# Kernel optimization log

Measured on AMD Instinct MI355X. Metric: run time of the kernel, lower is better.

## Reference

```python
import jax, jax.numpy as jnp
import numpy as np

N_NODES = 50000
N_EDGES = 800000
D = 64  # ndim_in = edim = n_hidden = n_out


def _glorot(key, shape):
    fan_in = shape[0]
    return jax.random.normal(key, shape, dtype=jnp.float32) / jnp.sqrt(jnp.float32(fan_in))


def setup_inputs() -> dict:
    key = jax.random.key(0)
    ks = jax.random.split(key, 10)
    return {
        "nfeats": jax.random.normal(ks[0], (N_NODES, D), dtype=jnp.float32),
        "efeats": jax.random.normal(ks[1], (N_EDGES, D), dtype=jnp.float32),
        "src": jax.random.randint(ks[2], (N_EDGES,), 0, N_NODES),
        "dst": jax.random.randint(ks[3], (N_EDGES,), 0, N_NODES),
        "wa0": _glorot(ks[4], (3 * D, D)), "ba0": jnp.zeros((D,), jnp.float32),
        "we0": _glorot(ks[5], (2 * D, D)), "be0": jnp.zeros((D,), jnp.float32),
        "wa1": _glorot(ks[6], (3 * D, D)), "ba1": jnp.zeros((D,), jnp.float32),
        "we1": _glorot(ks[7], (2 * D, D)), "be1": jnp.zeros((D,), jnp.float32),
    }


def _layer(h_nodes, h_edges, src, dst, wa, ba, we, be):
    n = h_nodes.shape[0]
    # per-edge message: concat(src node feat, edge feat)  [E, ndim+edim]
    msg = jnp.concatenate([h_nodes[src], h_edges], axis=1)
    # mean-reduce messages onto destination nodes (DGL fn.mean -> 0 if no in-edges)
    msum = jax.ops.segment_sum(msg, dst, num_segments=n)
    cnt = jax.ops.segment_sum(jnp.ones((msg.shape[0],), msg.dtype), dst, num_segments=n)
    h_neigh = msum / jnp.maximum(cnt, 1.0)[:, None]
    x_apply = jnp.concatenate([h_nodes, h_neigh], axis=1)  # [N, 2*ndim+edim]
    h_nodes_new = jax.nn.relu(x_apply @ wa + ba)
    # edge update: concat endpoint node outputs, then MLP
    edge_in = jnp.concatenate([h_nodes_new[src], h_nodes_new[dst]], axis=1)
    h_edges_new = jax.nn.relu(edge_in @ we + be)
    return h_nodes_new, h_edges_new


def reference(nfeats, efeats, src, dst, wa0, ba0, we0, be0, wa1, ba1, we1, be1):
    h_n, h_e = _layer(nfeats, efeats, src, dst, wa0, ba0, we0, be0)
    h_n, h_e = _layer(h_n, h_e, src, dst, wa1, ba1, we1, be1)
    return (h_n, h_e)
```

## Files before the change

kernel.cpp:

```cpp
#include <hip/hip_runtime.h>

#define NN 50000
#define NE 800000
#define CAP 64

typedef float f32x4 __attribute__((ext_vector_type(4)));
typedef unsigned short u16x4 __attribute__((ext_vector_type(4)));
typedef _Float16 f16x8 __attribute__((ext_vector_type(8)));

__device__ __forceinline__ float h_to_f(unsigned short u) {
    union { unsigned short s; _Float16 h; } c; c.s = u; return (float)c.h;
}
__device__ __forceinline__ unsigned short f_to_h(float f) {
    union { unsigned short s; _Float16 h; } c; c.h = (_Float16)f; return c.s;
}

__global__ __launch_bounds__(256) void k_prep(
    const float* __restrict__ nfeats, unsigned short* __restrict__ nfh)
{
    size_t b = ((size_t)blockIdx.x * 256 + threadIdx.x) * 4;
    f32x4 v = *(const f32x4*)(nfeats + b);
    u16x4 o;
#pragma unroll
    for (int j = 0; j < 4; ++j) o[j] = f_to_h(v[j]);
    *(u16x4*)(nfh + b) = o;
}

__global__ __launch_bounds__(256) void k_bucket(
    const int* __restrict__ src, const int* __restrict__ dst,
    int* __restrict__ fill, int2* __restrict__ epair)
{
    int e = blockIdx.x * 256 + threadIdx.x;
    int d = dst[e];
    int pos = atomicAdd(&fill[d], 1);
    if (pos < CAP) epair[(size_t)d * CAP + pos] = make_int2(src[e], e);
}

template <bool L2>
__global__ __launch_bounds__(256) void k_layer(
    const void* __restrict__ hin_,
    const unsigned short* __restrict__ nfh, const float* __restrict__ efeats,
    const unsigned short* __restrict__ P0g, const float* __restrict__ B0,
    const int* __restrict__ fill, const int2* __restrict__ epair,
    const float* __restrict__ wa, const float* __restrict__ ba,
    const float* __restrict__ we, const float* __restrict__ be,
    float* __restrict__ hout, unsigned short* __restrict__ pack,
    float* __restrict__ b32, unsigned short* __restrict__ a16,
    unsigned short* __restrict__ b16)
{
    __shared__ __align__(16) char smem[51200];
    __shared__ float ba_sh[64], be_sh[64];
    _Float16* xh  = (_Float16*)smem;
    _Float16* wah = (_Float16*)(smem + 25600);
    _Float16* heh = (_Float16*)smem;
    _Float16* weh = (_Float16*)(smem + 9216);

    int tid = threadIdx.x;
    int t0 = blockIdx.x * 64;
    if (tid < 64) { ba_sh[tid] = ba[tid]; be_sh[tid] = be[tid]; }

    for (int c = tid; c < 64 * 192; c += 256) {
        int n = c / 192, k = c - n * 192;
        wah[n * 200 + k] = (_Float16)wa[k * 64 + n];
    }
    for (int c = tid; c < 64 * 64; c += 256) {
        int rw = c >> 6, k = c & 63;
        int node = t0 + rw;
        float v = 0.f;
        if (node < NN) {
            if (L2) v = h_to_f(((const unsigned short*)hin_)[(size_t)node * 128 + k]);
            else    v = ((const float*)hin_)[(size_t)node * 64 + k];
        }
        xh[rw * 200 + k] = (_Float16)v;
    }

    int lane = tid & 63, wv = tid >> 6;
    for (int i = 0; i < 16; ++i) {
        int row = i * 4 + wv;
        int node = t0 + row;
        if (node >= NN) {
            xh[row * 200 + 64 + lane] = (_Float16)0.f;
            xh[row * 200 + 128 + lane] = (_Float16)0.f;
            continue;
        }
        int dg = fill[node];
        int nl = dg < CAP ? dg : CAP;
        int2 q = make_int2(0, 0);
        if (lane < nl) q = epair[(size_t)node * CAP + lane];
        float bB = 0.f;
        if (L2) bB = B0[(size_t)node * 64 + lane];
        float accN = 0.f, accE = 0.f;
        for (int t = 0; t < nl; t += 8) {
            int ss[8], ee[8];
#pragma unroll
            for (int u = 0; u < 8; ++u) {
                ss[u] = __shfl(q.x, t + u);
                ee[u] = __shfl(q.y, t + u);
            }
            float nv[8], ev[8];
#pragma unroll
            for (int u = 0; u < 8; ++u) {
                if (L2) {
                    nv[u] = h_to_f(P0g[(size_t)ss[u] * 128 + lane]);
                    ev[u] = h_to_f(P0g[(size_t)ss[u] * 128 + 64 + lane]);
                } else {
                    nv[u] = h_to_f(nfh[(size_t)ss[u] * 64 + lane]);
                    ev[u] = efeats[(size_t)ee[u] * 64 + lane];
                }
            }
#pragma unroll
            for (int u = 0; u < 8; ++u) {
                bool ok = (t + u) < nl;
                accN += ok ? nv[u] : 0.f;
                float x = L2 ? (ev[u] + bB) : ev[u];
                if (L2) x = x > 0.f ? x : 0.f;
                accE += ok ? x : 0.f;
            }
        }
        float dinv = 1.f / (float)(dg > 1 ? dg : 1);
        xh[row * 200 + 64 + lane]  = (_Float16)(accN * dinv);
        xh[row * 200 + 128 + lane] = (_Float16)(accE * dinv);
    }
    __syncthreads();

    int l15 = lane & 15, quad = lane >> 4;

    f32x4 acc[4];
#pragma unroll
    for (int nt = 0; nt < 4; ++nt) {
        float b = ba_sh[nt * 16 + l15];
        acc[nt] = (f32x4){b, b, b, b};
    }
    const _Float16* xp = xh + (wv * 16 + l15) * 200 + quad * 8;
    const _Float16* wp = wah + l15 * 200 + quad * 8;
#pragma unroll
    for (int ks = 0; ks < 6; ++ks) {
        f16x8 a  = *(const f16x8*)(xp + ks * 32);
        f16x8 b0 = *(const f16x8*)(wp + ks * 32);
        f16x8 b1 = *(const f16x8*)(wp + 16 * 200 + ks * 32);
        f16x8 b2 = *(const f16x8*)(wp + 32 * 200 + ks * 32);
        f16x8 b3 = *(const f16x8*)(wp + 48 * 200 + ks * 32);
        acc[0] = __builtin_amdgcn_mfma_f32_16x16x32_f16(a, b0, acc[0], 0, 0, 0);
        acc[1] = __builtin_amdgcn_mfma_f32_16x16x32_f16(a, b1, acc[1], 0, 0, 0);
        acc[2] = __builtin_amdgcn_mfma_f32_16x16x32_f16(a, b2, acc[2], 0, 0, 0);
        acc[3] = __builtin_amdgcn_mfma_f32_16x16x32_f16(a, b3, acc[3], 0, 0, 0);
    }
    __syncthreads();

    for (int c = tid; c < 8192; c += 256) {
        int n = c >> 6, k = c & 63;
        float wv_ = (n < 64) ? we[k * 64 + n] : we[(size_t)(64 + k) * 64 + (n - 64)];
        weh[n * 72 + k] = (_Float16)wv_;
    }
#pragma unroll
    for (int nt = 0; nt < 4; ++nt)
#pragma unroll
        for (int r = 0; r < 4; ++r) {
            float v = acc[nt][r];
            v = v > 0.f ? v : 0.f;
            int row = wv * 16 + quad * 4 + r, col = nt * 16 + l15;
            heh[row * 72 + col] = (_Float16)v;
            int node = t0 + row;
            if (node < NN) {
                if (L2) hout[(size_t)node * 64 + col] = v;
                else    pack[(size_t)node * 128 + col] = f_to_h(v);
            }
        }
    __syncthreads();

    f32x4 acc2[8];
#pragma unroll
    for (int nt = 0; nt < 8; ++nt) {
        float b = (nt >= 4) ? be_sh[(nt - 4) * 16 + l15] : 0.f;
        acc2[nt] = (f32x4){b, b, b, b};
    }
    const _Float16* hp = heh + (wv * 16 + l15) * 72 + quad * 8;
    const _Float16* vp = weh + l15 * 72 + quad * 8;
#pragma unroll
    for (int ks = 0; ks < 2; ++ks) {
        f16x8 a = *(const f16x8*)(hp + ks * 32);
#pragma unroll
        for (int nt = 0; nt < 8; ++nt) {
            f16x8 b = *(const f16x8*)(vp + nt * 16 * 72 + ks * 32);
            acc2[nt] = __builtin_amdgcn_mfma_f32_16x16x32_f16(a, b, acc2[nt], 0, 0, 0);
        }
    }
#pragma unroll
    for (int nt = 0; nt < 8; ++nt)
#pragma unroll
        for (int r = 0; r < 4; ++r) {
            float v = acc2[nt][r];
            int row = wv * 16 + quad * 4 + r, col = (nt & 3) * 16 + l15;
            int node = t0 + row;
            if (node < NN) {
                if (nt < 4) {
                    if (L2) a16[(size_t)node * 64 + col] = f_to_h(v);
                    else    pack[(size_t)node * 128 + 64 + col] = f_to_h(v);
                } else {
                    if (L2) b16[(size_t)node * 64 + col] = f_to_h(v);
                    else    b32[(size_t)node * 64 + col] = v;
                }
            }
        }
}

__global__ __launch_bounds__(256) void k_edge_out(
    const int* __restrict__ src, const int* __restrict__ dst,
    const unsigned short* __restrict__ A, const unsigned short* __restrict__ B,
    float* __restrict__ oute)
{
    size_t g = (size_t)blockIdx.x * 256 + threadIdx.x;
    size_t e = g >> 4;
    int c = ((int)g & 15) * 4;
    if (e >= NE) return;
    int s = src[e], d = dst[e];
    u16x4 a = *(const u16x4*)(A + (size_t)s * 64 + c);
    u16x4 b = *(const u16x4*)(B + (size_t)d * 64 + c);
    f32x4 v;
#pragma unroll
    for (int j = 0; j < 4; ++j) {
        float x = h_to_f(a[j]) + h_to_f(b[j]);
        v[j] = x > 0.f ? x : 0.f;
    }
    *(f32x4*)(oute + e * 64 + c) = v;
}

extern "C" void kernel_launch(void* const* d_in, const int* in_sizes, int n_in,
                              void* d_out, int out_size, void* d_ws, size_t ws_size,
                              hipStream_t stream)
{
    const float* nfeats = (const float*)d_in[0];
    const float* efeats = (const float*)d_in[1];
    const int*   src    = (const int*)d_in[2];
    const int*   dst    = (const int*)d_in[3];
    const float* wa0 = (const float*)d_in[4];
    const float* ba0 = (const float*)d_in[5];
    const float* we0 = (const float*)d_in[6];
    const float* be0 = (const float*)d_in[7];
    const float* wa1 = (const float*)d_in[8];
    const float* ba1 = (const float*)d_in[9];
    const float* we1 = (const float*)d_in[10];
    const float* be1 = (const float*)d_in[11];

    float* out_n = (float*)d_out;
    float* out_e = out_n + (size_t)NN * 64;

    char* w = (char*)d_ws;
    int* fill = (int*)w;  w += ((size_t)NN * 4 + 255) & ~(size_t)255;
    int2* epair = (int2*)w; w += (size_t)NN * CAP * 8;
    unsigned short* nfh = (unsigned short*)w; w += (size_t)NN * 64 * 2;
    unsigned short* P0  = (unsigned short*)w; w += (size_t)NN * 128 * 2;
    float* B0 = (float*)w; w += (size_t)NN * 64 * 4;
    unsigned short* A1 = (unsigned short*)w; w += (size_t)NN * 64 * 2;
    unsigned short* B1 = (unsigned short*)w; w += (size_t)NN * 64 * 2;

    hipMemsetAsync(fill, 0, (size_t)NN * 4, stream);
    k_prep<<<3125, 256, 0, stream>>>(nfeats, nfh);
    k_bucket<<<NE / 256, 256, 0, stream>>>(src, dst, fill, epair);

    k_layer<false><<<(NN + 63) / 64, 256, 0, stream>>>(
        nfeats, nfh, efeats, nullptr, nullptr, fill, epair,
        wa0, ba0, we0, be0, nullptr, P0, B0, nullptr, nullptr);

    k_layer<true><<<(NN + 63) / 64, 256, 0, stream>>>(
        P0, nullptr, nullptr, P0, B0, fill, epair,
        wa1, ba1, we1, be1, out_n, nullptr, nullptr, A1, B1);

    k_edge_out<<<(int)((size_t)NE * 16 / 256), 256, 0, stream>>>(src, dst, A1, B1, out_e);
}
```

Before: 685.9 us.

## Pre-convert weights once, bucket fp16 edge features by destination, shrink layer tiles

Adds a one-time weight prep kernel that transposes both layers' weights to fp16 in global memory. Layer kernels now read MFMA B operands straight from global memory instead of rebuilding them in LDS in every block. The bucket kernel now also scatters each edge's features, converted to fp16, into a per-destination contiguous buffer, so layer 0's aggregation reads contiguous rows instead of random fp32 rows. Node tiles shrink from 64 to 32 rows to reduce LDS use and increase block count, at the cost of a heavier bucketing pass and an extra ~400MB workspace write for the bucketed edges.

```diff
diff --git a/kernel.cpp b/kernel.cpp
--- a/kernel.cpp
+++ b/kernel.cpp
@@ -6,6 +6,7 @@
 
 typedef float f32x4 __attribute__((ext_vector_type(4)));
 typedef unsigned short u16x4 __attribute__((ext_vector_type(4)));
+typedef unsigned short u16x8 __attribute__((ext_vector_type(8)));
 typedef _Float16 f16x8 __attribute__((ext_vector_type(8)));
 
 __device__ __forceinline__ float h_to_f(unsigned short u) {
@@ -26,44 +27,71 @@
     *(u16x4*)(nfh + b) = o;
 }
 
+__global__ __launch_bounds__(256) void k_wprep(
+    const float* __restrict__ wa0, const float* __restrict__ we0,
+    const float* __restrict__ wa1, const float* __restrict__ we1,
+    _Float16* __restrict__ wahg, _Float16* __restrict__ wehg)
+{
+    int idx = blockIdx.x * 256 + threadIdx.x;
+    int layer = idx / 20480, r = idx % 20480;
+    const float* wa = layer ? wa1 : wa0;
+    const float* we = layer ? we1 : we0;
+    if (r < 12288) {
+        int n = r / 192, k = r % 192;
+        wahg[layer * 12288 + r] = (_Float16)wa[k * 64 + n];
+    } else {
+        int r2 = r - 12288;
+        int n = r2 >> 6, k = r2 & 63;
+        float v = (n < 64) ? we[k * 64 + n] : we[(size_t)(64 + k) * 64 + (n - 64)];
+        wehg[layer * 8192 + r2] = (_Float16)v;
+    }
+}
+
 __global__ __launch_bounds__(256) void k_bucket(
     const int* __restrict__ src, const int* __restrict__ dst,
-    int* __restrict__ fill, int2* __restrict__ epair)
+    const float* __restrict__ efeats, int* __restrict__ fill,
+    int* __restrict__ sbuck, unsigned short* __restrict__ ebuck)
 {
     int e = blockIdx.x * 256 + threadIdx.x;
     int d = dst[e];
     int pos = atomicAdd(&fill[d], 1);
-    if (pos < CAP) epair[(size_t)d * CAP + pos] = make_int2(src[e], e);
+    if (pos >= CAP) return;
+    size_t slot = (size_t)d * CAP + pos;
+    sbuck[slot] = src[e];
+    const float* er = efeats + (size_t)e * 64;
+    unsigned short* ew = ebuck + slot * 64;
+#pragma unroll
+    for (int j = 0; j < 8; ++j) {
+        f32x4 a = *(const f32x4*)(er + j * 8);
+        f32x4 b = *(const f32x4*)(er + j * 8 + 4);
+        u16x8 o;
+#pragma unroll
+        for (int q = 0; q < 4; ++q) { o[q] = f_to_h(a[q]); o[4 + q] = f_to_h(b[q]); }
+        *(u16x8*)(ew + j * 8) = o;
+    }
 }
 
 template <bool L2>
 __global__ __launch_bounds__(256) void k_layer(
     const void* __restrict__ hin_,
-    const unsigned short* __restrict__ nfh, const float* __restrict__ efeats,
+    const unsigned short* __restrict__ nfh, const unsigned short* __restrict__ ebuck,
     const unsigned short* __restrict__ P0g, const float* __restrict__ B0,
-    const int* __restrict__ fill, const int2* __restrict__ epair,
-    const float* __restrict__ wa, const float* __restrict__ ba,
-    const float* __restrict__ we, const float* __restrict__ be,
+    const int* __restrict__ fill, const int* __restrict__ sbuck,
+    const _Float16* __restrict__ wahg, const float* __restrict__ ba,
+    const _Float16* __restrict__ wehg, const float* __restrict__ be,
     float* __restrict__ hout, unsigned short* __restrict__ pack,
     float* __restrict__ b32, unsigned short* __restrict__ a16,
     unsigned short* __restrict__ b16)
 {
-    __shared__ __align__(16) char smem[51200];
+    __shared__ __align__(16) _Float16 xh[32 * 200];
+    _Float16* heh = xh;
     __shared__ float ba_sh[64], be_sh[64];
-    _Float16* xh  = (_Float16*)smem;
-    _Float16* wah = (_Float16*)(smem + 25600);
-    _Float16* heh = (_Float16*)smem;
-    _Float16* weh = (_Float16*)(smem + 9216);
 
     int tid = threadIdx.x;
-    int t0 = blockIdx.x * 64;
+    int t0 = blockIdx.x * 32;
     if (tid < 64) { ba_sh[tid] = ba[tid]; be_sh[tid] = be[tid]; }
 
-    for (int c = tid; c < 64 * 192; c += 256) {
-        int n = c / 192, k = c - n * 192;
-        wah[n * 200 + k] = (_Float16)wa[k * 64 + n];
-    }
-    for (int c = tid; c < 64 * 64; c += 256) {
+    for (int c = tid; c < 32 * 64; c += 256) {
         int rw = c >> 6, k = c & 63;
         int node = t0 + rw;
         float v = 0.f;
@@ -75,7 +103,7 @@
     }
 
     int lane = tid & 63, wv = tid >> 6;
-    for (int i = 0; i < 16; ++i) {
+    for (int i = 0; i < 8; ++i) {
         int row = i * 4 + wv;
         int node = t0 + row;
         if (node >= NN) {
@@ -85,18 +113,14 @@
         }
         int dg = fill[node];
         int nl = dg < CAP ? dg : CAP;
-        int2 q = make_int2(0, 0);
-        if (lane < nl) q = epair[(size_t)node * CAP + lane];
-        float bB = 0.f;
-        if (L2) bB = B0[(size_t)node * 64 + lane];
+        int sp = (lane < nl) ? sbuck[(size_t)node * CAP + lane] : 0;
+        float bB = L2 ? B0[(size_t)node * 64 + lane] : 0.f;
+        const unsigned short* eb = ebuck + (size_t)node * CAP * 64;
         float accN = 0.f, accE = 0.f;
         for (int t = 0; t < nl; t += 8) {
-            int ss[8], ee[8];
-#pragma unroll
-            for (int u = 0; u < 8; ++u) {
-                ss[u] = __shfl(q.x, t + u);
-                ee[u] = __shfl(q.y, t + u);
-            }
+            int ss[8];
+#pragma unroll
+            for (int u = 0; u < 8; ++u) ss[u] = __shfl(sp, t + u);
             float nv[8], ev[8];
 #pragma unroll
             for (int u = 0; u < 8; ++u) {
@@ -105,7 +129,7 @@
                     ev[u] = h_to_f(P0g[(size_t)ss[u] * 128 + 64 + lane]);
                 } else {
                     nv[u] = h_to_f(nfh[(size_t)ss[u] * 64 + lane]);
-                    ev[u] = efeats[(size_t)ee[u] * 64 + lane];
+                    ev[u] = h_to_f(eb[(size_t)(t + u) * 64 + lane]);
                 }
             }
 #pragma unroll
@@ -124,41 +148,34 @@
     __syncthreads();
 
     int l15 = lane & 15, quad = lane >> 4;
-
-    f32x4 acc[4];
-#pragma unroll
-    for (int nt = 0; nt < 4; ++nt) {
-        float b = ba_sh[nt * 16 + l15];
-        acc[nt] = (f32x4){b, b, b, b};
-    }
-    const _Float16* xp = xh + (wv * 16 + l15) * 200 + quad * 8;
-    const _Float16* wp = wah + l15 * 200 + quad * 8;
+    int mt = wv & 1, nh = wv >> 1;
+
+    f32x4 acc[2];
+#pragma unroll
+    for (int j = 0; j < 2; ++j) {
+        float b = ba_sh[(nh * 2 + j) * 16 + l15];
+        acc[j] = (f32x4){b, b, b, b};
+    }
+    const _Float16* xp  = xh + (mt * 16 + l15) * 200 + quad * 8;
+    const _Float16* wp0 = wahg + (size_t)((nh * 2 + 0) * 16 + l15) * 192 + quad * 8;
+    const _Float16* wp1 = wahg + (size_t)((nh * 2 + 1) * 16 + l15) * 192 + quad * 8;
 #pragma unroll
     for (int ks = 0; ks < 6; ++ks) {
         f16x8 a  = *(const f16x8*)(xp + ks * 32);
-        f16x8 b0 = *(const f16x8*)(wp + ks * 32);
-        f16x8 b1 = *(const f16x8*)(wp + 16 * 200 + ks * 32);
-        f16x8 b2 = *(const f16x8*)(wp + 32 * 200 + ks * 32);
-        f16x8 b3 = *(const f16x8*)(wp + 48 * 200 + ks * 32);
+        f16x8 b0 = *(const f16x8*)(wp0 + ks * 32);
+        f16x8 b1 = *(const f16x8*)(wp1 + ks * 32);
         acc[0] = __builtin_amdgcn_mfma_f32_16x16x32_f16(a, b0, acc[0], 0, 0, 0);
         acc[1] = __builtin_amdgcn_mfma_f32_16x16x32_f16(a, b1, acc[1], 0, 0, 0);
-        acc[2] = __builtin_amdgcn_mfma_f32_16x16x32_f16(a, b2, acc[2], 0, 0, 0);
-        acc[3] = __builtin_amdgcn_mfma_f32_16x16x32_f16(a, b3, acc[3], 0, 0, 0);
     }
     __syncthreads();
 
-    for (int c = tid; c < 8192; c += 256) {
-        int n = c >> 6, k = c & 63;
-        float wv_ = (n < 64) ? we[k * 64 + n] : we[(size_t)(64 + k) * 64 + (n - 64)];
-        weh[n * 72 + k] = (_Float16)wv_;
-    }
-#pragma unroll
-    for (int nt = 0; nt < 4; ++nt)
+#pragma unroll
+    for (int j = 0; j < 2; ++j)
 #pragma unroll
         for (int r = 0; r < 4; ++r) {
-            float v = acc[nt][r];
+            float v = acc[j][r];
             v = v > 0.f ? v : 0.f;
-            int row = wv * 16 + quad * 4 + r, col = nt * 16 + l15;
+            int row = mt * 16 + quad * 4 + r, col = (nh * 2 + j) * 16 + l15;
             heh[row * 72 + col] = (_Float16)v;
             int node = t0 + row;
             if (node < NN) {
@@ -168,35 +185,38 @@
         }
     __syncthreads();
 
-    f32x4 acc2[8];
-#pragma unroll
-    for (int nt = 0; nt < 8; ++nt) {
-        float b = (nt >= 4) ? be_sh[(nt - 4) * 16 + l15] : 0.f;
-        acc2[nt] = (f32x4){b, b, b, b};
-    }
-    const _Float16* hp = heh + (wv * 16 + l15) * 72 + quad * 8;
-    const _Float16* vp = weh + l15 * 72 + quad * 8;
+    f32x4 acc2[4];
+#pragma unroll
+    for (int j = 0; j < 4; ++j) {
+        int col128 = (nh * 4 + j) * 16 + l15;
+        float b = (col128 >= 64) ? be_sh[col128 - 64] : 0.f;
+        acc2[j] = (f32x4){b, b, b, b};
+    }
+    const _Float16* hp = heh + (mt * 16 + l15) * 72 + quad * 8;
 #pragma unroll
     for (int ks = 0; ks < 2; ++ks) {
         f16x8 a = *(const f16x8*)(hp + ks * 32);
 #pragma unroll
-        for (int nt = 0; nt < 8; ++nt) {
-            f16x8 b = *(const f16x8*)(vp + nt * 16 * 72 + ks * 32);
-            acc2[nt] = __builtin_amdgcn_mfma_f32_16x16x32_f16(a, b, acc2[nt], 0, 0, 0);
-        }
-    }
-#pragma unroll
-    for (int nt = 0; nt < 8; ++nt)
+        for (int j = 0; j < 4; ++j) {
+            const _Float16* vp = wehg + (size_t)((nh * 4 + j) * 16 + l15) * 64 + ks * 32 + quad * 8;
+            f16x8 b = *(const f16x8*)vp;
+            acc2[j] = __builtin_amdgcn_mfma_f32_16x16x32_f16(a, b, acc2[j], 0, 0, 0);
+        }
+    }
+#pragma unroll
+    for (int j = 0; j < 4; ++j)
 #pragma unroll
         for (int r = 0; r < 4; ++r) {
-            float v = acc2[nt][r];
-            int row = wv * 16 + quad * 4 + r, col = (nt & 3) * 16 + l15;
+            float v = acc2[j][r];
+            int row = mt * 16 + quad * 4 + r;
+            int col128 = (nh * 4 + j) * 16 + l15;
             int node = t0 + row;
             if (node < NN) {
-                if (nt < 4) {
-                    if (L2) a16[(size_t)node * 64 + col] = f_to_h(v);
-                    else    pack[(size_t)node * 128 + 64 + col] = f_to_h(v);
+                if (col128 < 64) {
+                    if (L2) a16[(size_t)node * 64 + col128] = f_to_h(v);
+                    else    pack[(size_t)node * 128 + 64 + col128] = f_to_h(v);
                 } else {
+                    int col = col128 - 64;
                     if (L2) b16[(size_t)node * 64 + col] = f_to_h(v);
                     else    b32[(size_t)node * 64 + col] = v;
                 }
@@ -247,24 +267,28 @@
 
     char* w = (char*)d_ws;
     int* fill = (int*)w;  w += ((size_t)NN * 4 + 255) & ~(size_t)255;
-    int2* epair = (int2*)w; w += (size_t)NN * CAP * 8;
+    int* sbuck = (int*)w; w += (size_t)NN * CAP * 4;
+    unsigned short* ebuck = (unsigned short*)w; w += (size_t)NN * CAP * 128;
     unsigned short* nfh = (unsigned short*)w; w += (size_t)NN * 64 * 2;
     unsigned short* P0  = (unsigned short*)w; w += (size_t)NN * 128 * 2;
     float* B0 = (float*)w; w += (size_t)NN * 64 * 4;
     unsigned short* A1 = (unsigned short*)w; w += (size_t)NN * 64 * 2;
     unsigned short* B1 = (unsigned short*)w; w += (size_t)NN * 64 * 2;
+    _Float16* wahg = (_Float16*)w; w += 2 * 12288 * 2;
+    _Float16* wehg = (_Float16*)w;
 
     hipMemsetAsync(fill, 0, (size_t)NN * 4, stream);
     k_prep<<<3125, 256, 0, stream>>>(nfeats, nfh);
-    k_bucket<<<NE / 256, 256, 0, stream>>>(src, dst, fill, epair);
-
-    k_layer<false><<<(NN + 63) / 64, 256, 0, stream>>>(
-        nfeats, nfh, efeats, nullptr, nullptr, fill, epair,
-        wa0, ba0, we0, be0, nullptr, P0, B0, nullptr, nullptr);
-
-    k_layer<true><<<(NN + 63) / 64, 256, 0, stream>>>(
-        P0, nullptr, nullptr, P0, B0, fill, epair,
-        wa1, ba1, we1, be1, out_n, nullptr, nullptr, A1, B1);
+    k_wprep<<<160, 256, 0, stream>>>(wa0, we0, wa1, we1, wahg, wehg);
+    k_bucket<<<NE / 256, 256, 0, stream>>>(src, dst, efeats, fill, sbuck, ebuck);
+
+    k_layer<false><<<(NN + 31) / 32, 256, 0, stream>>>(
+        nfeats, nfh, ebuck, nullptr, nullptr, fill, sbuck,
+        wahg, ba0, wehg, be0, nullptr, P0, B0, nullptr, nullptr);
+
+    k_layer<true><<<(NN + 31) / 32, 256, 0, stream>>>(
+        P0, nullptr, nullptr, P0, B0, fill, sbuck,
+        wahg + 12288, ba1, wehg + 8192, be1, out_n, nullptr, nullptr, A1, B1);
 
     k_edge_out<<<(int)((size_t)NE * 16 / 256), 256, 0, stream>>>(src, dst, A1, B1, out_e);
 }
```

New measurement: 624.8 us. 8.9% less time.
